# Optimization experiments

Hardware: AMD Instinct MI355X
Metric: run time of the kernel (lower is better)

The kernel has to match this reference:

```python
import jax, jax.numpy as jnp
import numpy as np

C = 51  # num_relation


def setup_inputs() -> dict:
    key = jax.random.key(0)
    N_o, N_u, D = 16384, 16384, 1024
    k = jax.random.split(key, 6)
    feat = jax.random.normal(k[0], (N_o + N_u, D), jnp.float32)
    # first N_o rows are labeled (label != 0), remaining N_u rows unlabeled (label == 0)
    label = jnp.concatenate([
        jax.random.randint(k[1], (N_o,), 1, C),
        jnp.zeros((N_u,), jnp.int32),
    ]).astype(jnp.int32)
    W_o = jax.random.normal(k[2], (C, D), jnp.float32) * 0.03
    b_o = jnp.zeros((C,), jnp.float32)
    W = jax.random.normal(k[3], (C, D), jnp.float32) * 0.03
    b = jnp.zeros((C,), jnp.float32)
    cls = jnp.arange(C)
    group_mid_mask = (cls >= 16) & (cls < 36)   # groups[1]
    group_tail_mask = cls >= 36                 # groups[2]
    # runtime torch.randint partner sampling, hoisted to input construction
    idx_m = jax.random.randint(k[4], (2, N_u), 0, N_o)  # 2 mid copies
    idx_t = jax.random.randint(k[5], (3, N_u), 0, N_o)  # 3 tail copies
    return dict(feat=feat, label=label, W_o=W_o, b_o=b_o, W=W, b=b,
                group_mid_mask=group_mid_mask, group_tail_mask=group_tail_mask,
                idx_m=idx_m, idx_t=idx_t)


def reference(feat, label, W_o, b_o, W, b, group_mid_mask, group_tail_mask, idx_m, idx_t):
    n_u = idx_m.shape[1]
    n_o = feat.shape[0] - n_u
    feat_o, feat_u = feat[:n_o], feat[n_o:]
    label_o = label[:n_o]

    # fc_o under no_grad, then softmax / top-1 rank + score
    logits = jax.lax.stop_gradient(feat_u @ W_o.T + b_o)      # [N_u, C]
    p = jax.nn.softmax(logits, axis=1)
    pred = jnp.argmax(p, axis=1)                               # ranks[:,0]
    score = jnp.max(p, axis=1)                                 # score[:,0]

    # group membership + confidence thresholds (heads are unused in the original)
    mid_m = group_mid_mask[pred] & (score > 0.5)
    tail_m = group_tail_mask[pred] & (score > 0.3)

    oh_u = jax.nn.one_hot(pred, C, dtype=feat.dtype)
    oh_o = jax.nn.one_hot(label_o, C, dtype=feat.dtype)

    im = idx_m.reshape(-1)   # [2*N_u]
    it = idx_t.reshape(-1)   # [3*N_u]

    fm = 0.7 * feat_o[im] + 0.3 * jnp.tile(feat_u, (2, 1))
    lm = 0.7 * oh_o[im] + 0.3 * jnp.tile(oh_u, (2, 1))
    ft = 0.7 * feat_o[it] + 0.3 * jnp.tile(feat_u, (3, 1))
    lt = 0.7 * oh_o[it] + 0.3 * jnp.tile(oh_u, (3, 1))

    feat_cat = jnp.concatenate([fm, ft], axis=0)               # [5*N_u, D]
    label_cat = jnp.concatenate([lm, lt], axis=0)              # [5*N_u, C]
    w = jnp.concatenate([jnp.tile(mid_m, 2), jnp.tile(tail_m, 3)]).astype(feat.dtype)

    # soft-label cross entropy on fc(feat_cat); masked mean over selected rows
    logp = jax.nn.log_softmax(feat_cat @ W.T + b, axis=1)
    ce = -(logp * label_cat).sum(axis=1)
    cnt = w.sum()
    return (ce * w).sum() / jnp.maximum(cnt, 1.0)
```

## Files before the change

kernel.cpp:

```cpp
#include <hip/hip_runtime.h>
#include <math.h>

#define DD 1024
#define SN 52
#define NU 16384
#define NO 16384

typedef short short8 __attribute__((ext_vector_type(8)));
typedef float f32x4 __attribute__((ext_vector_type(4)));

__device__ __forceinline__ unsigned short f2b(float x) {
    unsigned int u = __float_as_uint(x);
    u += 0x7FFFu + ((u >> 16) & 1u);
    return (unsigned short)(u >> 16);
}

__device__ __forceinline__ uint4 pack8(float4 a, float4 b) {
    uint4 r;
    r.x = (unsigned)f2b(a.x) | ((unsigned)f2b(a.y) << 16);
    r.y = (unsigned)f2b(a.z) | ((unsigned)f2b(a.w) << 16);
    r.z = (unsigned)f2b(b.x) | ((unsigned)f2b(b.y) << 16);
    r.w = (unsigned)f2b(b.z) | ((unsigned)f2b(b.w) << 16);
    return r;
}

__global__ __launch_bounds__(256) void convW(const float* __restrict__ W,
                                             const float* __restrict__ W_o,
                                             unsigned short* __restrict__ Wcat) {
    const int n = blockIdx.x;
    const int k = threadIdx.x * 4;
    const float* src = nullptr;
    if (n < 64) { if (n < 51) src = W + (size_t)n * DD; }
    else        { if (n - 64 < 51) src = W_o + (size_t)(n - 64) * DD; }
    float4 v = src ? *(const float4*)(src + k) : make_float4(0.f, 0.f, 0.f, 0.f);
    ushort4 o;
    o.x = f2b(v.x); o.y = f2b(v.y); o.z = f2b(v.z); o.w = f2b(v.w);
    *(ushort4*)(Wcat + (size_t)n * DD + k) = o;
}

template <int NFR>
__device__ __forceinline__ void gemm_body(const float* __restrict__ feat,
                                          const unsigned short* __restrict__ Wcat,
                                          unsigned short* As, unsigned short* Bs,
                                          int m0, float* __restrict__ Bmat,
                                          float* __restrict__ Lmat) {
    const int tid = threadIdx.x;
    const int lane = tid & 63;
    const int w = tid >> 6;
    const int col16 = lane & 15;
    const int quad = lane >> 4;
    const int ar = tid >> 2, aq = tid & 3;
    const int bn = tid >> 1, bh = tid & 1;
    const float* aptr = feat + (size_t)(m0 + ar) * DD + aq * 16;
    const unsigned short* bptr =
        (bn < NFR * 16) ? Wcat + (size_t)bn * DD + bh * 32 : nullptr;

    f32x4 acc[NFR];
#pragma unroll
    for (int nf = 0; nf < NFR; ++nf) acc[nf] = (f32x4){0.f, 0.f, 0.f, 0.f};

    for (int k0 = 0; k0 < DD; k0 += 64) {
        const float4* asrc = (const float4*)(aptr + k0);
        float4 a0 = asrc[0], a1 = asrc[1], a2 = asrc[2], a3 = asrc[3];
        uint4 b0, b1, b2, b3;
        if (bptr) {
            const uint4* bsrc = (const uint4*)(bptr + k0);
            b0 = bsrc[0]; b1 = bsrc[1]; b2 = bsrc[2]; b3 = bsrc[3];
        }
        __syncthreads();
        uint4* ad = (uint4*)(As + ar * 72 + aq * 16);
        ad[0] = pack8(a0, a1);
        ad[1] = pack8(a2, a3);
        if (bptr) {
            uint4* bd = (uint4*)(Bs + bn * 72 + bh * 32);
            bd[0] = b0; bd[1] = b1; bd[2] = b2; bd[3] = b3;
        }
        __syncthreads();
#pragma unroll
        for (int kk = 0; kk < 64; kk += 32) {
            short8 af = *(const short8*)(As + (w * 16 + col16) * 72 + kk + quad * 8);
#pragma unroll
            for (int nf = 0; nf < NFR; ++nf) {
                short8 bf = *(const short8*)(Bs + (nf * 16 + col16) * 72 + kk + quad * 8);
                acc[nf] = __builtin_amdgcn_mfma_f32_16x16x32_bf16(af, bf, acc[nf], 0, 0, 0);
            }
        }
    }

    const int rbase = m0 + w * 16 + quad * 4;
#pragma unroll
    for (int nf = 0; nf < NFR; ++nf) {
        const int colL = nf * 16 + col16;
#pragma unroll
        for (int r = 0; r < 4; ++r) {
            const float v = acc[nf][r];
            const int row = rbase + r;
            if (colL < 51) {
                Bmat[(size_t)row * SN + colL] = v;
            } else if (NFR == 8 && colL >= 64 && colL - 64 < 51) {
                Lmat[(size_t)(row - NO) * SN + (colL - 64)] = v;
            }
        }
    }
}

__global__ __launch_bounds__(256) void gemm_mfma(const float* __restrict__ feat,
                                                 const unsigned short* __restrict__ Wcat,
                                                 float* __restrict__ Bmat,
                                                 float* __restrict__ Lmat) {
    __shared__ unsigned short As[64 * 72];
    __shared__ unsigned short Bs[128 * 72];
    const int m0 = blockIdx.x * 64;
    if (m0 < NO) gemm_body<4>(feat, Wcat, As, Bs, m0, Bmat, Lmat);
    else         gemm_body<8>(feat, Wcat, As, Bs, m0, Bmat, Lmat);
}

__global__ __launch_bounds__(256) void decide(const float* __restrict__ L,
                                              const float* __restrict__ b_o,
                                              int* __restrict__ flags) {
    const int w = threadIdx.x >> 6;
    const int lane = threadIdx.x & 63;
    const int row = blockIdx.x * 4 + w;
    float z = -INFINITY;
    if (lane < 51) z = L[(size_t)row * SN + lane] + b_o[lane];
    float m = z;
    int mi = lane;
#pragma unroll
    for (int off = 1; off < 64; off <<= 1) {
        float om = __shfl_xor(m, off);
        int oi = __shfl_xor(mi, off);
        if (om > m || (om == m && oi < mi)) { m = om; mi = oi; }
    }
    float e = (lane < 51) ? expf(z - m) : 0.f;
#pragma unroll
    for (int off = 1; off < 64; off <<= 1) e += __shfl_xor(e, off);
    const float score = 1.f / e;
    const int mid = (mi >= 16 && mi < 36 && score > 0.5f) ? 1 : 0;
    const int tail = (mi >= 36 && score > 0.3f) ? 1 : 0;
    if (lane == 0) flags[row] = mi | (mid << 8) | (tail << 9);
}

__global__ __launch_bounds__(256) void cekernel(const float* __restrict__ B,
                                                const float* __restrict__ bb,
                                                const int* __restrict__ label,
                                                const int* __restrict__ idxm,
                                                const int* __restrict__ idxt,
                                                const int* __restrict__ flags,
                                                double* __restrict__ gnum,
                                                int* __restrict__ gcnt) {
    __shared__ double snum[4];
    __shared__ int scnt[4];
    const int w = threadIdx.x >> 6;
    const int lane = threadIdx.x & 63;
    const int j = blockIdx.x * 4 + w;
    int u, o, active;
    if (j < 2 * NU) {
        u = j & (NU - 1);
        o = idxm[j];
        active = (flags[u] >> 8) & 1;
    } else {
        const int j2 = j - 2 * NU;
        u = j2 & (NU - 1);
        o = idxt[j2];
        active = (flags[u] >> 9) & 1;
    }
    float ce = 0.f;
    if (active) {
        const float* Bo = B + (size_t)o * SN;
        const float* Bu = B + (size_t)(NO + u) * SN;
        float z = -INFINITY;
        if (lane < 51) z = 0.7f * Bo[lane] + 0.3f * Bu[lane] + bb[lane];
        float m = z;
#pragma unroll
        for (int off = 1; off < 64; off <<= 1) m = fmaxf(m, __shfl_xor(m, off));
        float e = (lane < 51) ? expf(z - m) : 0.f;
#pragma unroll
        for (int off = 1; off < 64; off <<= 1) e += __shfl_xor(e, off);
        const float lse = m + logf(e);
        const int lo = label[o];
        const int pu = flags[u] & 255;
        const float zlo = __shfl(z, lo);
        const float zpu = __shfl(z, pu);
        ce = lse - 0.7f * zlo - 0.3f * zpu;
    }
    if (lane == 0) { snum[w] = (double)ce; scnt[w] = active; }
    __syncthreads();
    if (threadIdx.x == 0) {
        const double n = snum[0] + snum[1] + snum[2] + snum[3];
        const int c = scnt[0] + scnt[1] + scnt[2] + scnt[3];
        if (c > 0) {
            atomicAdd(gnum, n);
            atomicAdd(gcnt, c);
        }
    }
}

__global__ void finalize(const double* __restrict__ gnum,
                         const int* __restrict__ gcnt,
                         float* __restrict__ out) {
    if (threadIdx.x == 0 && blockIdx.x == 0) {
        const double c = (double)(*gcnt);
        out[0] = (float)(*gnum / (c > 1.0 ? c : 1.0));
    }
}

extern "C" void kernel_launch(void* const* d_in, const int* in_sizes, int n_in,
                              void* d_out, int out_size, void* d_ws, size_t ws_size,
                              hipStream_t stream) {
    const float* feat = (const float*)d_in[0];
    const int* label = (const int*)d_in[1];
    const float* W_o = (const float*)d_in[2];
    const float* b_o = (const float*)d_in[3];
    const float* W = (const float*)d_in[4];
    const float* b = (const float*)d_in[5];
    const int* idxm = (const int*)d_in[8];
    const int* idxt = (const int*)d_in[9];

    float* ws = (float*)d_ws;
    float* Bmat = ws;
    float* Lmat = Bmat + (size_t)(NO + NU) * SN;
    int* flags = (int*)(Lmat + (size_t)NU * SN);
    char* accb = (char*)(flags + NU);
    double* gnum = (double*)accb;
    int* gcnt = (int*)(accb + 8);
    unsigned short* Wcat = (unsigned short*)(accb + 16);

    hipMemsetAsync(accb, 0, 16, stream);
    convW<<<128, 256, 0, stream>>>(W, W_o, Wcat);
    gemm_mfma<<<(NO + NU) / 64, 256, 0, stream>>>(feat, Wcat, Bmat, Lmat);
    decide<<<NU / 4, 256, 0, stream>>>(Lmat, b_o, flags);
    cekernel<<<(5 * NU) / 4, 256, 0, stream>>>(Bmat, b, label, idxm, idxt, flags, gnum, gcnt);
    finalize<<<1, 64, 0, stream>>>(gnum, gcnt, (float*)d_out);
}
```

Measured before the change: 235.3 us.

## Drop LDS staging in GEMM, fuse decide into epilogue, replace atomics with partials

The GEMM now has each wave load its A rows and B fragments straight from global memory into registers, with register double-buffering, instead of staging them through shared memory behind barriers. The softmax/argmax decision for unlabeled rows is computed in the GEMM epilogue, which removes the separate decide kernel and the Lmat round trip. The CE kernel writes per-block partial sums rather than doing global atomics, and a 256-thread finalize reduces them, which also drops the memset. B fragments are now reloaded from global/L2 by every wave with no LDS reuse.

```diff
diff --git a/kernel.cpp b/kernel.cpp
--- a/kernel.cpp
+++ b/kernel.cpp
@@ -5,6 +5,7 @@
 #define SN 52
 #define NU 16384
 #define NO 16384
+#define CEBLK 20480
 
 typedef short short8 __attribute__((ext_vector_type(8)));
 typedef float f32x4 __attribute__((ext_vector_type(4)));
@@ -15,12 +16,12 @@
     return (unsigned short)(u >> 16);
 }
 
-__device__ __forceinline__ uint4 pack8(float4 a, float4 b) {
-    uint4 r;
-    r.x = (unsigned)f2b(a.x) | ((unsigned)f2b(a.y) << 16);
-    r.y = (unsigned)f2b(a.z) | ((unsigned)f2b(a.w) << 16);
-    r.z = (unsigned)f2b(b.x) | ((unsigned)f2b(b.y) << 16);
-    r.w = (unsigned)f2b(b.z) | ((unsigned)f2b(b.w) << 16);
+__device__ __forceinline__ short8 cvt8(float4 a, float4 b) {
+    short8 r;
+    r[0] = (short)f2b(a.x); r[1] = (short)f2b(a.y);
+    r[2] = (short)f2b(a.z); r[3] = (short)f2b(a.w);
+    r[4] = (short)f2b(b.x); r[5] = (short)f2b(b.y);
+    r[6] = (short)f2b(b.z); r[7] = (short)f2b(b.w);
     return r;
 }
 
@@ -39,105 +40,105 @@
 }
 
 template <int NFR>
-__device__ __forceinline__ void gemm_body(const float* __restrict__ feat,
+__device__ __forceinline__ void gemm_wave(const float* __restrict__ feat,
                                           const unsigned short* __restrict__ Wcat,
-                                          unsigned short* As, unsigned short* Bs,
+                                          const float* __restrict__ b_o,
                                           int m0, float* __restrict__ Bmat,
-                                          float* __restrict__ Lmat) {
-    const int tid = threadIdx.x;
-    const int lane = tid & 63;
-    const int w = tid >> 6;
+                                          int* __restrict__ flags) {
+    const int lane = threadIdx.x & 63;
+    const int w = threadIdx.x >> 6;
     const int col16 = lane & 15;
     const int quad = lane >> 4;
-    const int ar = tid >> 2, aq = tid & 3;
-    const int bn = tid >> 1, bh = tid & 1;
-    const float* aptr = feat + (size_t)(m0 + ar) * DD + aq * 16;
-    const unsigned short* bptr =
-        (bn < NFR * 16) ? Wcat + (size_t)bn * DD + bh * 32 : nullptr;
+    const float* ap = feat + (size_t)(m0 + w * 16 + col16) * DD + quad * 8;
+    const unsigned short* bp = Wcat + (size_t)col16 * DD + quad * 8;
 
     f32x4 acc[NFR];
 #pragma unroll
     for (int nf = 0; nf < NFR; ++nf) acc[nf] = (f32x4){0.f, 0.f, 0.f, 0.f};
 
-    for (int k0 = 0; k0 < DD; k0 += 64) {
-        const float4* asrc = (const float4*)(aptr + k0);
-        float4 a0 = asrc[0], a1 = asrc[1], a2 = asrc[2], a3 = asrc[3];
-        uint4 b0, b1, b2, b3;
-        if (bptr) {
-            const uint4* bsrc = (const uint4*)(bptr + k0);
-            b0 = bsrc[0]; b1 = bsrc[1]; b2 = bsrc[2]; b3 = bsrc[3];
-        }
-        __syncthreads();
-        uint4* ad = (uint4*)(As + ar * 72 + aq * 16);
-        ad[0] = pack8(a0, a1);
-        ad[1] = pack8(a2, a3);
-        if (bptr) {
-            uint4* bd = (uint4*)(Bs + bn * 72 + bh * 32);
-            bd[0] = b0; bd[1] = b1; bd[2] = b2; bd[3] = b3;
-        }
-        __syncthreads();
-#pragma unroll
-        for (int kk = 0; kk < 64; kk += 32) {
-            short8 af = *(const short8*)(As + (w * 16 + col16) * 72 + kk + quad * 8);
-#pragma unroll
-            for (int nf = 0; nf < NFR; ++nf) {
-                short8 bf = *(const short8*)(Bs + (nf * 16 + col16) * 72 + kk + quad * 8);
-                acc[nf] = __builtin_amdgcn_mfma_f32_16x16x32_bf16(af, bf, acc[nf], 0, 0, 0);
+    float4 a0 = ((const float4*)ap)[0];
+    float4 a1 = ((const float4*)ap)[1];
+    short8 bf[NFR];
+#pragma unroll
+    for (int nf = 0; nf < NFR; ++nf)
+        bf[nf] = *(const short8*)(bp + (size_t)nf * 16 * DD);
+
+    for (int k0 = 32; k0 <= DD; k0 += 32) {
+        float4 na0, na1;
+        short8 nbf[NFR];
+        if (k0 < DD) {
+            na0 = ((const float4*)(ap + k0))[0];
+            na1 = ((const float4*)(ap + k0))[1];
+#pragma unroll
+            for (int nf = 0; nf < NFR; ++nf)
+                nbf[nf] = *(const short8*)(bp + (size_t)nf * 16 * DD + k0);
+        }
+        const short8 af = cvt8(a0, a1);
+#pragma unroll
+        for (int nf = 0; nf < NFR; ++nf)
+            acc[nf] = __builtin_amdgcn_mfma_f32_16x16x32_bf16(af, bf[nf], acc[nf], 0, 0, 0);
+        a0 = na0; a1 = na1;
+#pragma unroll
+        for (int nf = 0; nf < NFR; ++nf) bf[nf] = nbf[nf];
+    }
+
+    const int rbase = m0 + w * 16 + quad * 4;
+#pragma unroll
+    for (int nf = 0; nf < 4; ++nf) {
+        const int colL = nf * 16 + col16;
+        if (colL < 51) {
+#pragma unroll
+            for (int r = 0; r < 4; ++r)
+                Bmat[(size_t)(rbase + r) * SN + colL] = acc[nf][r];
+        }
+    }
+    if constexpr (NFR == 8) {
+        float boc[4];
+#pragma unroll
+        for (int c = 0; c < 4; ++c) {
+            const int col = c * 16 + col16;
+            boc[c] = (col < 51) ? b_o[col] : 0.f;
+        }
+#pragma unroll
+        for (int r = 0; r < 4; ++r) {
+            float z[4];
+            float m = acc[4][r] + boc[0];
+            int mi = col16;
+            z[0] = m;
+#pragma unroll
+            for (int c = 1; c < 4; ++c) {
+                const int col = c * 16 + col16;
+                z[c] = (col < 51) ? acc[4 + c][r] + boc[c] : -INFINITY;
+                if (z[c] > m) { m = z[c]; mi = col; }
             }
-        }
-    }
-
-    const int rbase = m0 + w * 16 + quad * 4;
-#pragma unroll
-    for (int nf = 0; nf < NFR; ++nf) {
-        const int colL = nf * 16 + col16;
-#pragma unroll
-        for (int r = 0; r < 4; ++r) {
-            const float v = acc[nf][r];
-            const int row = rbase + r;
-            if (colL < 51) {
-                Bmat[(size_t)row * SN + colL] = v;
-            } else if (NFR == 8 && colL >= 64 && colL - 64 < 51) {
-                Lmat[(size_t)(row - NO) * SN + (colL - 64)] = v;
+#pragma unroll
+            for (int off = 1; off < 16; off <<= 1) {
+                const float om = __shfl_xor(m, off);
+                const int oi = __shfl_xor(mi, off);
+                if (om > m || (om == m && oi < mi)) { m = om; mi = oi; }
             }
+            float e = 0.f;
+#pragma unroll
+            for (int c = 0; c < 4; ++c)
+                if (c * 16 + col16 < 51) e += expf(z[c] - m);
+#pragma unroll
+            for (int off = 1; off < 16; off <<= 1) e += __shfl_xor(e, off);
+            const float score = 1.f / e;
+            const int mid = (mi >= 16 && mi < 36 && score > 0.5f) ? 1 : 0;
+            const int tail = (mi >= 36 && score > 0.3f) ? 1 : 0;
+            if (col16 == 0) flags[rbase + r - NO] = mi | (mid << 8) | (tail << 9);
         }
     }
 }
 
 __global__ __launch_bounds__(256) void gemm_mfma(const float* __restrict__ feat,
                                                  const unsigned short* __restrict__ Wcat,
+                                                 const float* __restrict__ b_o,
                                                  float* __restrict__ Bmat,
-                                                 float* __restrict__ Lmat) {
-    __shared__ unsigned short As[64 * 72];
-    __shared__ unsigned short Bs[128 * 72];
+                                                 int* __restrict__ flags) {
     const int m0 = blockIdx.x * 64;
-    if (m0 < NO) gemm_body<4>(feat, Wcat, As, Bs, m0, Bmat, Lmat);
-    else         gemm_body<8>(feat, Wcat, As, Bs, m0, Bmat, Lmat);
-}
-
-__global__ __launch_bounds__(256) void decide(const float* __restrict__ L,
-                                              const float* __restrict__ b_o,
-                                              int* __restrict__ flags) {
-    const int w = threadIdx.x >> 6;
-    const int lane = threadIdx.x & 63;
-    const int row = blockIdx.x * 4 + w;
-    float z = -INFINITY;
-    if (lane < 51) z = L[(size_t)row * SN + lane] + b_o[lane];
-    float m = z;
-    int mi = lane;
-#pragma unroll
-    for (int off = 1; off < 64; off <<= 1) {
-        float om = __shfl_xor(m, off);
-        int oi = __shfl_xor(mi, off);
-        if (om > m || (om == m && oi < mi)) { m = om; mi = oi; }
-    }
-    float e = (lane < 51) ? expf(z - m) : 0.f;
-#pragma unroll
-    for (int off = 1; off < 64; off <<= 1) e += __shfl_xor(e, off);
-    const float score = 1.f / e;
-    const int mid = (mi >= 16 && mi < 36 && score > 0.5f) ? 1 : 0;
-    const int tail = (mi >= 36 && score > 0.3f) ? 1 : 0;
-    if (lane == 0) flags[row] = mi | (mid << 8) | (tail << 9);
+    if (m0 < NO) gemm_wave<4>(feat, Wcat, b_o, m0, Bmat, flags);
+    else         gemm_wave<8>(feat, Wcat, b_o, m0, Bmat, flags);
 }
 
 __global__ __launch_bounds__(256) void cekernel(const float* __restrict__ B,
@@ -146,9 +147,9 @@
                                                 const int* __restrict__ idxm,
                                                 const int* __restrict__ idxt,
                                                 const int* __restrict__ flags,
-                                                double* __restrict__ gnum,
-                                                int* __restrict__ gcnt) {
-    __shared__ double snum[4];
+                                                double* __restrict__ pnum,
+                                                int* __restrict__ pcnt) {
+    __shared__ float snum[4];
     __shared__ int scnt[4];
     const int w = threadIdx.x >> 6;
     const int lane = threadIdx.x & 63;
@@ -183,24 +184,39 @@
         const float zpu = __shfl(z, pu);
         ce = lse - 0.7f * zlo - 0.3f * zpu;
     }
-    if (lane == 0) { snum[w] = (double)ce; scnt[w] = active; }
+    if (lane == 0) { snum[w] = ce; scnt[w] = active; }
     __syncthreads();
     if (threadIdx.x == 0) {
-        const double n = snum[0] + snum[1] + snum[2] + snum[3];
-        const int c = scnt[0] + scnt[1] + scnt[2] + scnt[3];
-        if (c > 0) {
-            atomicAdd(gnum, n);
-            atomicAdd(gcnt, c);
-        }
-    }
-}
-
-__global__ void finalize(const double* __restrict__ gnum,
-                         const int* __restrict__ gcnt,
-                         float* __restrict__ out) {
-    if (threadIdx.x == 0 && blockIdx.x == 0) {
-        const double c = (double)(*gcnt);
-        out[0] = (float)(*gnum / (c > 1.0 ? c : 1.0));
+        pnum[blockIdx.x] = (double)snum[0] + (double)snum[1] +
+                           (double)snum[2] + (double)snum[3];
+        pcnt[blockIdx.x] = scnt[0] + scnt[1] + scnt[2] + scnt[3];
+    }
+}
+
+__global__ __launch_bounds__(256) void finalize(const double* __restrict__ pnum,
+                                                const int* __restrict__ pcnt,
+                                                float* __restrict__ out) {
+    __shared__ double sd[4];
+    __shared__ int sc[4];
+    const int w = threadIdx.x >> 6;
+    const int lane = threadIdx.x & 63;
+    double s = 0.0;
+    int c = 0;
+    for (int i = threadIdx.x; i < CEBLK; i += 256) {
+        s += pnum[i];
+        c += pcnt[i];
+    }
+#pragma unroll
+    for (int off = 1; off < 64; off <<= 1) {
+        s += __shfl_xor(s, off);
+        c += __shfl_xor(c, off);
+    }
+    if (lane == 0) { sd[w] = s; sc[w] = c; }
+    __syncthreads();
+    if (threadIdx.x == 0) {
+        const double n = sd[0] + sd[1] + sd[2] + sd[3];
+        const int cc = sc[0] + sc[1] + sc[2] + sc[3];
+        out[0] = (float)(n / (cc > 1 ? (double)cc : 1.0));
     }
 }
 
@@ -216,19 +232,16 @@
     const int* idxm = (const int*)d_in[8];
     const int* idxt = (const int*)d_in[9];
 
-    float* ws = (float*)d_ws;
-    float* Bmat = ws;
-    float* Lmat = Bmat + (size_t)(NO + NU) * SN;
-    int* flags = (int*)(Lmat + (size_t)NU * SN);
-    char* accb = (char*)(flags + NU);
-    double* gnum = (double*)accb;
-    int* gcnt = (int*)(accb + 8);
-    unsigned short* Wcat = (unsigned short*)(accb + 16);
-
-    hipMemsetAsync(accb, 0, 16, stream);
+    char* ws = (char*)d_ws;
+    float* Bmat = (float*)ws;
+    double* pnum = (double*)(ws + 6815744);
+    int* pcnt = (int*)(ws + 6815744 + 163840);
+    int* flags = (int*)(ws + 6815744 + 163840 + 81920);
+    unsigned short* Wcat =
+        (unsigned short*)(ws + 6815744 + 163840 + 81920 + 65536);
+
     convW<<<128, 256, 0, stream>>>(W, W_o, Wcat);
-    gemm_mfma<<<(NO + NU) / 64, 256, 0, stream>>>(feat, Wcat, Bmat, Lmat);
-    decide<<<NU / 4, 256, 0, stream>>>(Lmat, b_o, flags);
-    cekernel<<<(5 * NU) / 4, 256, 0, stream>>>(Bmat, b, label, idxm, idxt, flags, gnum, gcnt);
-    finalize<<<1, 64, 0, stream>>>(gnum, gcnt, (float*)d_out);
-}
+    gemm_mfma<<<(NO + NU) / 64, 256, 0, stream>>>(feat, Wcat, b_o, Bmat, flags);
+    cekernel<<<CEBLK, 256, 0, stream>>>(Bmat, b, label, idxm, idxt, flags, pnum, pcnt);
+    finalize<<<1, 256, 0, stream>>>(pnum, pcnt, (float*)d_out);
+}
```

After: 274.9 us. +16.8%, slower.
